# Kernel tuning notes

Hardware: AMD Instinct MI355X
Metric: run time of the kernel (lower is better)

The kernel has to match this reference:

```python
import jax, jax.numpy as jnp
import numpy as np
import math

B, N, E, D = 4, 8192, 1024, 64

def setup_inputs() -> dict:
    key = jax.random.key(0)
    kx, kq, kk, kv, ko = jax.random.split(key, 5)
    x = jax.random.normal(kx, (B, N, E), dtype=jnp.float32)
    # ImplicitLinear weights: hash-generated Rademacher-like values scaled by 1/sqrt(in_features).
    # We stand in with sign(normal) * scale, matching the statistics of v_mask_generative * scale.
    wq = jnp.sign(jax.random.normal(kq, (D, E), dtype=jnp.float32)) / math.sqrt(E)
    wk = jnp.sign(jax.random.normal(kk, (D, E), dtype=jnp.float32)) / math.sqrt(E)
    wv = jnp.sign(jax.random.normal(kv, (D, E), dtype=jnp.float32)) / math.sqrt(E)
    wo = jnp.sign(jax.random.normal(ko, (E, D), dtype=jnp.float32)) / math.sqrt(D)
    return {"x": x, "wq": wq, "wk": wk, "wv": wv, "wo": wo}

def reference(x, wq, wk, wv, wo):
    # Projections: ImplicitLinear computes x @ W.T with W shaped [out, in]
    Q = jnp.einsum('bne,de->bnd', x, wq)   # [B,N,D]
    K = jnp.einsum('bne,de->bnd', x, wk)   # [B,N,D]
    V = jnp.einsum('bne,de->bnd', x, wv)   # [B,N,D]
    # ground mode: linear attention, energy = K^T @ V  -> [B,D,D]
    energy = jnp.einsum('bnd,bne->bde', K, V)
    context = jnp.einsum('bnd,bde->bne', Q, energy)  # [B,N,D]
    context = context * jnp.asarray(math.sqrt(3.0 / D), dtype=context.dtype)
    out = jnp.einsum('bnd,ed->bne', context, wo)  # [B,N,E]
    return out
```

## Files before the change

### kernel.cpp

```cpp
#include <hip/hip_runtime.h>
#include <hip/hip_bf16.h>
#include <stdint.h>


typedef __bf16 bf16x8 __attribute__((ext_vector_type(8)));
typedef float  f32x4  __attribute__((ext_vector_type(4)));

#define MFMA_BF16(A, Bb, C) __builtin_amdgcn_mfma_f32_16x16x32_bf16(A, Bb, C, 0, 0, 0)

__global__ __launch_bounds__(128) void prep_kernel(
    const float* __restrict__ wq, const float* __restrict__ wk,
    const float* __restrict__ wv, const float* __restrict__ wo,
    __bf16* __restrict__ Wb)
{
    const int gid = blockIdx.x * 128 + threadIdx.x;
    const int e0  = gid * 8;
    const float* src = (e0 < 65536)  ? wq + e0
                     : (e0 < 131072) ? wk + (e0 - 65536)
                     : (e0 < 196608) ? wv + (e0 - 131072)
                                     : wo + (e0 - 196608);
    float w[8];
    *(float4*)&w[0] = *(const float4*)(src);
    *(float4*)&w[4] = *(const float4*)(src + 4);
    bf16x8 wb;
#pragma unroll
    for (int j = 0; j < 8; ++j) wb[j] = (__bf16)w[j];
    *(bf16x8*)&Wb[e0] = wb;
}

__global__ __launch_bounds__(256) void qkv_kernel(
    const float* __restrict__ x, const __bf16* __restrict__ Wb,
    float* __restrict__ Qf, float* __restrict__ Kf, float* __restrict__ Vf)
{
    const int tid  = threadIdx.x;
    const int lane = tid & 63;
    const int wid  = tid >> 6;
    const int lr   = lane & 15;
    const int kg   = lane >> 4;
    const int slab = blockIdx.x >> 1;
    const int c0   = (blockIdx.x & 1) * 96;
    const int row0 = slab * 64 + wid * 16;

    const float* xrow = &x[(size_t)(row0 + lr) * 1024 + kg * 8];

    f32x4 acc[6];
#pragma unroll
    for (int i = 0; i < 6; ++i) acc[i] = (f32x4){0.f, 0.f, 0.f, 0.f};

    float4 pa0, pa1, qa0, qa1;
    bf16x8 Bc[6], Bn[6];

#define LOAD_A(B0, B1, STP) {                                                  \
        const float* ap_ = xrow + (STP) * 32;                                  \
        B0 = *(const float4*)(ap_);                                            \
        B1 = *(const float4*)(ap_ + 4); }
#define LOAD_B(BARR, STP) {                                                    \
        _Pragma("unroll")                                                      \
        for (int bn_ = 0; bn_ < 6; ++bn_)                                      \
            BARR[bn_] = *(const bf16x8*)&Wb[(size_t)(c0 + bn_ * 16 + lr) * 1024 \
                                            + (STP) * 32 + kg * 8]; }
#define K1_STEP(S, A0_, A1_, BC, BN) {                                         \
        if ((S) + 1 < 32) LOAD_B(BN, (S) + 1);                                 \
        bf16x8 Ah_, Al_;                                                       \
        const float* fp_ = (const float*)&A0_;                                 \
        _Pragma("unroll")                                                      \
        for (int j_ = 0; j_ < 4; ++j_) {                                       \
            const unsigned int bb_ = __float_as_uint(fp_[j_]);                 \
            Ah_[j_] = __builtin_bit_cast(__bf16, (unsigned short)(bb_ >> 16)); \
            Al_[j_] = (__bf16)(fp_[j_] - __uint_as_float(bb_ & 0xffff0000u));  \
        }                                                                      \
        const float* gp_ = (const float*)&A1_;                                 \
        _Pragma("unroll")                                                      \
        for (int j_ = 0; j_ < 4; ++j_) {                                       \
            const unsigned int bb_ = __float_as_uint(gp_[j_]);                 \
            Ah_[4 + j_] = __builtin_bit_cast(__bf16, (unsigned short)(bb_ >> 16)); \
            Al_[4 + j_] = (__bf16)(gp_[j_] - __uint_as_float(bb_ & 0xffff0000u)); \
        }                                                                      \
        if ((S) + 2 < 32) LOAD_A(A0_, A1_, (S) + 2);                           \
        _Pragma("unroll")                                                      \
        for (int bn_ = 0; bn_ < 6; ++bn_) {                                    \
            acc[bn_] = MFMA_BF16(Ah_, BC[bn_], acc[bn_]);                      \
            acc[bn_] = MFMA_BF16(Al_, BC[bn_], acc[bn_]);                      \
        } }

    LOAD_A(pa0, pa1, 0);
    LOAD_A(qa0, qa1, 1);
    LOAD_B(Bc, 0);

    for (int s = 0; s < 32; s += 2) {
        K1_STEP(s,     pa0, pa1, Bc, Bn);
        K1_STEP(s + 1, qa0, qa1, Bn, Bc);
    }
#undef LOAD_A
#undef LOAD_B
#undef K1_STEP

#pragma unroll
    for (int bn = 0; bn < 6; ++bn) {
        const int col  = c0 + bn * 16 + lr;
        const int rowb = row0 + kg * 4;
        float* dst = (col < 64) ? Qf : (col < 128) ? Kf : Vf;
        const int cc = col & 63;
#pragma unroll
        for (int r = 0; r < 4; ++r)
            dst[(size_t)(rowb + r) * 64 + cc] = acc[bn][r];
    }
}

__global__ __launch_bounds__(256) void energy_partial_kernel(
    const float* __restrict__ Kf, const float* __restrict__ Vf,
    float* __restrict__ part)
{
    __shared__ float lK[64 * 64];
    __shared__ float lV[64 * 64];
    const int tid  = threadIdx.x;
    const int row0 = blockIdx.x * 64;

#pragma unroll
    for (int i = 0; i < 4; ++i) {
        const int idx = tid + i * 256;
        const int r   = idx >> 4;
        const int c4  = (idx & 15) << 2;
        *(float4*)&lK[r * 64 + c4] = *(const float4*)&Kf[(size_t)(row0 + r) * 64 + c4];
        *(float4*)&lV[r * 64 + c4] = *(const float4*)&Vf[(size_t)(row0 + r) * 64 + c4];
    }
    __syncthreads();

    const int d  = tid & 63;
    const int eb = (tid >> 6) * 16;
    float acc[16];
#pragma unroll
    for (int j = 0; j < 16; ++j) acc[j] = 0.f;

    for (int n = 0; n < 64; ++n) {
        const float kd = lK[n * 64 + d];
        const float4 v0 = *(const float4*)&lV[n * 64 + eb];
        const float4 v1 = *(const float4*)&lV[n * 64 + eb + 4];
        const float4 v2 = *(const float4*)&lV[n * 64 + eb + 8];
        const float4 v3 = *(const float4*)&lV[n * 64 + eb + 12];
        acc[0]  += kd * v0.x; acc[1]  += kd * v0.y; acc[2]  += kd * v0.z; acc[3]  += kd * v0.w;
        acc[4]  += kd * v1.x; acc[5]  += kd * v1.y; acc[6]  += kd * v1.z; acc[7]  += kd * v1.w;
        acc[8]  += kd * v2.x; acc[9]  += kd * v2.y; acc[10] += kd * v2.z; acc[11] += kd * v2.w;
        acc[12] += kd * v3.x; acc[13] += kd * v3.y; acc[14] += kd * v3.z; acc[15] += kd * v3.w;
    }
    float* p = part + (size_t)blockIdx.x * 4096 + d * 64 + eb;
#pragma unroll
    for (int i = 0; i < 4; ++i)
        *(float4*)&p[i * 4] = make_float4(acc[i*4], acc[i*4+1], acc[i*4+2], acc[i*4+3]);
}

__global__ __launch_bounds__(256) void energy_reduce_kernel(
    const float* __restrict__ part, __bf16* __restrict__ Eth, __bf16* __restrict__ Etl)
{
    const int b    = blockIdx.x >> 4;
    const int elem = ((blockIdx.x & 15) << 8) + threadIdx.x;
    float s = 0.f;
#pragma unroll 8
    for (int c = 0; c < 128; ++c)
        s += part[(size_t)(b * 128 + c) * 4096 + elem];
    s *= 0.2165063509461097f;
    const int d = elem >> 6, e = elem & 63;
    const __bf16 h = (__bf16)s;
    const __bf16 l = (__bf16)(s - (float)h);
    const size_t o = (size_t)b * 4096 + e * 64 + d;
    Eth[o] = h; Etl[o] = l;
}

__global__ __launch_bounds__(256) void out_kernel(
    const float* __restrict__ Qf,
    const __bf16* __restrict__ Eth, const __bf16* __restrict__ Etl,
    const __bf16* __restrict__ Wob, float* __restrict__ out)
{
    __shared__ float ct[4][16 * 68];

    const int tid  = threadIdx.x;
    const int lane = tid & 63;
    const int wid  = tid >> 6;
    const int lr   = lane & 15;
    const int kg   = lane >> 4;
    const int slab = blockIdx.x >> 1;
    const int c0   = (blockIdx.x & 1) * 512;
    const int row0 = slab * 64 + wid * 16;
    const int b    = blockIdx.x >> 8;

    bf16x8 Qh[2], Ql[2];
#pragma unroll
    for (int ks = 0; ks < 2; ++ks) {
        float qv[8];
        const float* src = &Qf[(size_t)(row0 + lr) * 64 + ks * 32 + kg * 8];
        *(float4*)&qv[0] = *(const float4*)(src);
        *(float4*)&qv[4] = *(const float4*)(src + 4);
#pragma unroll
        for (int j = 0; j < 8; ++j) {
            const unsigned int bb = __float_as_uint(qv[j]);
            Qh[ks][j] = __builtin_bit_cast(__bf16, (unsigned short)(bb >> 16));
            Ql[ks][j] = (__bf16)(qv[j] - __uint_as_float(bb & 0xffff0000u));
        }
    }

    f32x4 cacc[4];
#pragma unroll
    for (int i = 0; i < 4; ++i) cacc[i] = (f32x4){0.f, 0.f, 0.f, 0.f};
#pragma unroll
    for (int ks = 0; ks < 2; ++ks) {
#pragma unroll
        for (int eb = 0; eb < 4; ++eb) {
            const int e = eb * 16 + lr;
            const bf16x8 Bh = *(const bf16x8*)&Eth[(size_t)b * 4096 + e * 64 + ks * 32 + kg * 8];
            const bf16x8 Bl = *(const bf16x8*)&Etl[(size_t)b * 4096 + e * 64 + ks * 32 + kg * 8];
            cacc[eb] = MFMA_BF16(Qh[ks], Bh, cacc[eb]);
            cacc[eb] = MFMA_BF16(Qh[ks], Bl, cacc[eb]);
            cacc[eb] = MFMA_BF16(Ql[ks], Bh, cacc[eb]);
        }
    }

#pragma unroll
    for (int eb = 0; eb < 4; ++eb)
#pragma unroll
        for (int r = 0; r < 4; ++r)
            ct[wid][(kg * 4 + r) * 68 + eb * 16 + lr] = cacc[eb][r];
    asm volatile("s_waitcnt lgkmcnt(0)" ::: "memory");

    bf16x8 Ah[2], Al[2];
#pragma unroll
    for (int ks = 0; ks < 2; ++ks) {
        float f[8];
#pragma unroll
        for (int i = 0; i < 2; ++i)
            *(float4*)&f[i * 4] = *(const float4*)&ct[wid][lr * 68 + ks * 32 + kg * 8 + i * 4];
#pragma unroll
        for (int j = 0; j < 8; ++j) {
            const unsigned int bb = __float_as_uint(f[j]);
            Ah[ks][j] = __builtin_bit_cast(__bf16, (unsigned short)(bb >> 16));
            Al[ks][j] = (__bf16)(f[j] - __uint_as_float(bb & 0xffff0000u));
        }
    }

    for (int g = 0; g < 8; ++g) {
        f32x4 oacc[4];
#pragma unroll
        for (int i = 0; i < 4; ++i) oacc[i] = (f32x4){0.f, 0.f, 0.f, 0.f};
#pragma unroll
        for (int ks = 0; ks < 2; ++ks) {
#pragma unroll
            for (int bn = 0; bn < 4; ++bn) {
                const int col = c0 + g * 64 + bn * 16 + lr;
                const bf16x8 Bw = *(const bf16x8*)&Wob[(size_t)col * 64 + ks * 32 + kg * 8];
                oacc[bn] = MFMA_BF16(Ah[ks], Bw, oacc[bn]);
                oacc[bn] = MFMA_BF16(Al[ks], Bw, oacc[bn]);
            }
        }
#pragma unroll
        for (int bn = 0; bn < 4; ++bn)
#pragma unroll
            for (int r = 0; r < 4; ++r)
                __builtin_nontemporal_store(oacc[bn][r],
                    &out[(size_t)(row0 + kg * 4 + r) * 1024 + c0 + g * 64 + bn * 16 + lr]);
    }
}

extern "C" void kernel_launch(void* const* d_in, const int* in_sizes, int n_in,
                              void* d_out, int out_size, void* d_ws, size_t ws_size,
                              hipStream_t stream)
{
    const float* x  = (const float*)d_in[0];
    const float* wq = (const float*)d_in[1];
    const float* wk = (const float*)d_in[2];
    const float* wv = (const float*)d_in[3];
    const float* wo = (const float*)d_in[4];
    float* out = (float*)d_out;

    char* ws = (char*)d_ws;
    float*  Qf   = (float*)(ws);
    float*  Kf   = (float*)(ws + 8388608);
    float*  Vf   = (float*)(ws + 16777216);
    float*  part = (float*)(ws + 25165824);
    __bf16* Wb   = (__bf16*)(ws + 33554432);
    __bf16* Wob  = Wb + 196608;
    __bf16* Eth  = (__bf16*)(ws + 34603008);
    __bf16* Etl  = (__bf16*)(ws + 34635776);

    prep_kernel<<<256, 128, 0, stream>>>(wq, wk, wv, wo, Wb);
    qkv_kernel<<<1024, 256, 0, stream>>>(x, Wb, Qf, Kf, Vf);
    energy_partial_kernel<<<512, 256, 0, stream>>>(Kf, Vf, part);
    energy_reduce_kernel<<<64, 256, 0, stream>>>(part, Eth, Etl);
    out_kernel<<<1024, 256, 0, stream>>>(Qf, Eth, Etl, Wob, out);
}
```

Baseline: 362.5 us.

## Precompose energy with output weights and stage x tiles through LDS in QKV

```diff
diff --git a/kernel.cpp b/kernel.cpp
--- a/kernel.cpp
+++ b/kernel.cpp
@@ -4,9 +4,25 @@
 
 
 typedef __bf16 bf16x8 __attribute__((ext_vector_type(8)));
+typedef __bf16 bf16x4 __attribute__((ext_vector_type(4)));
 typedef float  f32x4  __attribute__((ext_vector_type(4)));
 
 #define MFMA_BF16(A, Bb, C) __builtin_amdgcn_mfma_f32_16x16x32_bf16(A, Bb, C, 0, 0, 0)
+
+__device__ __forceinline__ void gload_lds16(const void* g, void* l) {
+    __builtin_amdgcn_global_load_lds(
+        (const __attribute__((address_space(1))) unsigned int*)g,
+        (__attribute__((address_space(3))) unsigned int*)l, 16, 0, 0);
+}
+
+__device__ __forceinline__ void split8(const float* f, bf16x8& h, bf16x8& l) {
+#pragma unroll
+    for (int j = 0; j < 8; ++j) {
+        const unsigned int u = __float_as_uint(f[j]);
+        h[j] = __builtin_bit_cast(__bf16, (unsigned short)(u >> 16));
+        l[j] = (__bf16)(f[j] - __uint_as_float(u & 0xffff0000u));
+    }
+}
 
 __global__ __launch_bounds__(128) void prep_kernel(
     const float* __restrict__ wq, const float* __restrict__ wk,
@@ -28,82 +44,83 @@
     *(bf16x8*)&Wb[e0] = wb;
 }
 
-__global__ __launch_bounds__(256) void qkv_kernel(
+__global__ __launch_bounds__(512, 4) void qkv_kernel(
     const float* __restrict__ x, const __bf16* __restrict__ Wb,
     float* __restrict__ Qf, float* __restrict__ Kf, float* __restrict__ Vf)
 {
+    __shared__ float xt[2][64 * 64];
+
     const int tid  = threadIdx.x;
     const int lane = tid & 63;
     const int wid  = tid >> 6;
     const int lr   = lane & 15;
     const int kg   = lane >> 4;
-    const int slab = blockIdx.x >> 1;
-    const int c0   = (blockIdx.x & 1) * 96;
-    const int row0 = slab * 64 + wid * 16;
-
-    const float* xrow = &x[(size_t)(row0 + lr) * 1024 + kg * 8];
+    const int wr   = wid >> 1;
+    const int wc   = wid & 1;
+    const int row0 = blockIdx.x * 64;
+
+    const int q0 = wid * 2;
+    const int s0 = q0 * 64 + lane;
+    const int s1 = s0 + 64;
+    const int r0 = s0 >> 4, c0 = s0 & 15;
+    const int r1 = s1 >> 4, c1 = s1 & 15;
+    const float* src0 = x + (size_t)(row0 + r0) * 1024 + (c0 ^ (r0 & 7)) * 4;
+    const float* src1 = x + (size_t)(row0 + r1) * 1024 + (c1 ^ (r1 & 7)) * 4;
+
+#define STAGE(stp, buf) {                                                      \
+        gload_lds16(src0 + (stp) * 64, (char*)&xt[buf][0] + (q0 + 0) * 1024);  \
+        gload_lds16(src1 + (stp) * 64, (char*)&xt[buf][0] + (q0 + 1) * 1024); }
 
     f32x4 acc[6];
 #pragma unroll
     for (int i = 0; i < 6; ++i) acc[i] = (f32x4){0.f, 0.f, 0.f, 0.f};
 
-    float4 pa0, pa1, qa0, qa1;
-    bf16x8 Bc[6], Bn[6];
-
-#define LOAD_A(B0, B1, STP) {                                                  \
-        const float* ap_ = xrow + (STP) * 32;                                  \
-        B0 = *(const float4*)(ap_);                                            \
-        B1 = *(const float4*)(ap_ + 4); }
-#define LOAD_B(BARR, STP) {                                                    \
-        _Pragma("unroll")                                                      \
-        for (int bn_ = 0; bn_ < 6; ++bn_)                                      \
-            BARR[bn_] = *(const bf16x8*)&Wb[(size_t)(c0 + bn_ * 16 + lr) * 1024 \
-                                            + (STP) * 32 + kg * 8]; }
-#define K1_STEP(S, A0_, A1_, BC, BN) {                                         \
-        if ((S) + 1 < 32) LOAD_B(BN, (S) + 1);                                 \
-        bf16x8 Ah_, Al_;                                                       \
-        const float* fp_ = (const float*)&A0_;                                 \
-        _Pragma("unroll")                                                      \
-        for (int j_ = 0; j_ < 4; ++j_) {                                       \
-            const unsigned int bb_ = __float_as_uint(fp_[j_]);                 \
-            Ah_[j_] = __builtin_bit_cast(__bf16, (unsigned short)(bb_ >> 16)); \
-            Al_[j_] = (__bf16)(fp_[j_] - __uint_as_float(bb_ & 0xffff0000u));  \
-        }                                                                      \
-        const float* gp_ = (const float*)&A1_;                                 \
-        _Pragma("unroll")                                                      \
-        for (int j_ = 0; j_ < 4; ++j_) {                                       \
-            const unsigned int bb_ = __float_as_uint(gp_[j_]);                 \
-            Ah_[4 + j_] = __builtin_bit_cast(__bf16, (unsigned short)(bb_ >> 16)); \
-            Al_[4 + j_] = (__bf16)(gp_[j_] - __uint_as_float(bb_ & 0xffff0000u)); \
-        }                                                                      \
-        if ((S) + 2 < 32) LOAD_A(A0_, A1_, (S) + 2);                           \
-        _Pragma("unroll")                                                      \
-        for (int bn_ = 0; bn_ < 6; ++bn_) {                                    \
-            acc[bn_] = MFMA_BF16(Ah_, BC[bn_], acc[bn_]);                      \
-            acc[bn_] = MFMA_BF16(Al_, BC[bn_], acc[bn_]);                      \
-        } }
-
-    LOAD_A(pa0, pa1, 0);
-    LOAD_A(qa0, qa1, 1);
-    LOAD_B(Bc, 0);
-
-    for (int s = 0; s < 32; s += 2) {
-        K1_STEP(s,     pa0, pa1, Bc, Bn);
-        K1_STEP(s + 1, qa0, qa1, Bn, Bc);
-    }
-#undef LOAD_A
-#undef LOAD_B
-#undef K1_STEP
-
-#pragma unroll
-    for (int bn = 0; bn < 6; ++bn) {
-        const int col  = c0 + bn * 16 + lr;
-        const int rowb = row0 + kg * 4;
+    STAGE(0, 0);
+
+    const int ar  = wr * 16 + lr;
+    const int am  = ar & 7;
+
+    for (int step = 0; step < 16; ++step) {
+        const int cur = step & 1;
+        __syncthreads();
+
+        bf16x8 Bw[2][6];
+#pragma unroll
+        for (int ks = 0; ks < 2; ++ks)
+#pragma unroll
+            for (int n = 0; n < 6; ++n)
+                Bw[ks][n] = *(const bf16x8*)&Wb[(size_t)(wc * 96 + n * 16 + lr) * 1024
+                                                + step * 64 + ks * 32 + kg * 8];
+        if (step + 1 < 16) STAGE(step + 1, cur ^ 1);
+
+        bf16x8 Ah[2], Al[2];
+#pragma unroll
+        for (int ks = 0; ks < 2; ++ks) {
+            const int g0 = ks * 8 + kg * 2;
+            float f[8];
+            *(f32x4*)&f[0] = *(const f32x4*)&xt[cur][ar * 64 + ((g0    ) ^ am) * 4];
+            *(f32x4*)&f[4] = *(const f32x4*)&xt[cur][ar * 64 + ((g0 + 1) ^ am) * 4];
+            split8(f, Ah[ks], Al[ks]);
+        }
+#pragma unroll
+        for (int ks = 0; ks < 2; ++ks)
+#pragma unroll
+            for (int n = 0; n < 6; ++n) {
+                acc[n] = MFMA_BF16(Ah[ks], Bw[ks][n], acc[n]);
+                acc[n] = MFMA_BF16(Al[ks], Bw[ks][n], acc[n]);
+            }
+    }
+#undef STAGE
+
+#pragma unroll
+    for (int n = 0; n < 6; ++n) {
+        const int col  = wc * 96 + n * 16 + lr;
+        const int rowb = row0 + wr * 16 + kg * 4;
         float* dst = (col < 64) ? Qf : (col < 128) ? Kf : Vf;
         const int cc = col & 63;
 #pragma unroll
         for (int r = 0; r < 4; ++r)
-            dst[(size_t)(rowb + r) * 64 + cc] = acc[bn][r];
+            dst[(size_t)(rowb + r) * 64 + cc] = acc[n][r];
     }
 }
 
@@ -150,7 +167,7 @@
 }
 
 __global__ __launch_bounds__(256) void energy_reduce_kernel(
-    const float* __restrict__ part, __bf16* __restrict__ Eth, __bf16* __restrict__ Etl)
+    const float* __restrict__ part, __bf16* __restrict__ Eh, __bf16* __restrict__ El)
 {
     const int b    = blockIdx.x >> 4;
     const int elem = ((blockIdx.x & 15) << 8) + threadIdx.x;
@@ -159,103 +176,127 @@
     for (int c = 0; c < 128; ++c)
         s += part[(size_t)(b * 128 + c) * 4096 + elem];
     s *= 0.2165063509461097f;
-    const int d = elem >> 6, e = elem & 63;
     const __bf16 h = (__bf16)s;
     const __bf16 l = (__bf16)(s - (float)h);
-    const size_t o = (size_t)b * 4096 + e * 64 + d;
-    Eth[o] = h; Etl[o] = l;
-}
-
-__global__ __launch_bounds__(256) void out_kernel(
-    const float* __restrict__ Qf,
-    const __bf16* __restrict__ Eth, const __bf16* __restrict__ Etl,
-    const __bf16* __restrict__ Wob, float* __restrict__ out)
-{
-    __shared__ float ct[4][16 * 68];
-
+    Eh[b * 4096 + elem] = h;
+    El[b * 4096 + elem] = l;
+}
+
+__global__ __launch_bounds__(256) void f_kernel(
+    const __bf16* __restrict__ Eh, const __bf16* __restrict__ El,
+    const __bf16* __restrict__ Wob,
+    __bf16* __restrict__ Fth, __bf16* __restrict__ Ftl)
+{
     const int tid  = threadIdx.x;
     const int lane = tid & 63;
     const int wid  = tid >> 6;
     const int lr   = lane & 15;
     const int kg   = lane >> 4;
-    const int slab = blockIdx.x >> 1;
-    const int c0   = (blockIdx.x & 1) * 512;
-    const int row0 = slab * 64 + wid * 16;
-    const int b    = blockIdx.x >> 8;
+    const int b    = blockIdx.x >> 2;
+    const int cg   = blockIdx.x & 3;
+
+    bf16x8 Ah[2], Al[2];
+#pragma unroll
+    for (int ks = 0; ks < 2; ++ks) {
+        const size_t o = (size_t)b * 4096 + (wid * 16 + lr) * 64 + ks * 32 + kg * 8;
+        Ah[ks] = *(const bf16x8*)&Eh[o];
+        Al[ks] = *(const bf16x8*)&El[o];
+    }
+
+#pragma unroll
+    for (int grp = 0; grp < 4; ++grp) {
+        f32x4 acc[4];
+#pragma unroll
+        for (int i = 0; i < 4; ++i) acc[i] = (f32x4){0.f, 0.f, 0.f, 0.f};
+        bf16x8 Bw[4][2];
+#pragma unroll
+        for (int n = 0; n < 4; ++n)
+#pragma unroll
+            for (int ks = 0; ks < 2; ++ks) {
+                const int col = cg * 256 + grp * 64 + n * 16 + lr;
+                Bw[n][ks] = *(const bf16x8*)&Wob[(size_t)col * 64 + ks * 32 + kg * 8];
+            }
+#pragma unroll
+        for (int ks = 0; ks < 2; ++ks)
+#pragma unroll
+            for (int n = 0; n < 4; ++n) {
+                acc[n] = MFMA_BF16(Ah[ks], Bw[n][ks], acc[n]);
+                acc[n] = MFMA_BF16(Al[ks], Bw[n][ks], acc[n]);
+            }
+#pragma unroll
+        for (int n = 0; n < 4; ++n) {
+            const int col = cg * 256 + grp * 64 + n * 16 + lr;
+            bf16x4 hv, lv;
+#pragma unroll
+            for (int r = 0; r < 4; ++r) {
+                const float v = acc[n][r];
+                hv[r] = (__bf16)v;
+                lv[r] = (__bf16)(v - (float)hv[r]);
+            }
+            const size_t o = (size_t)b * 65536 + (size_t)col * 64 + wid * 16 + kg * 4;
+            *(bf16x4*)&Fth[o] = hv;
+            *(bf16x4*)&Ftl[o] = lv;
+        }
+    }
+}
+
+__global__ __launch_bounds__(256, 4) void out_kernel(
+    const float* __restrict__ Qf,
+    const __bf16* __restrict__ Fth, const __bf16* __restrict__ Ftl,
+    float* __restrict__ out)
+{
+    const int tid    = threadIdx.x;
+    const int lane   = tid & 63;
+    const int wid    = tid >> 6;
+    const int lr     = lane & 15;
+    const int kg     = lane >> 4;
+    const int rowblk = blockIdx.x >> 2;
+    const int cg     = blockIdx.x & 3;
+    const int row0   = rowblk * 64 + wid * 16;
+    const int b      = rowblk >> 7;
 
     bf16x8 Qh[2], Ql[2];
-#pragma unroll
-    for (int ks = 0; ks < 2; ++ks) {
-        float qv[8];
-        const float* src = &Qf[(size_t)(row0 + lr) * 64 + ks * 32 + kg * 8];
-        *(float4*)&qv[0] = *(const float4*)(src);
-        *(float4*)&qv[4] = *(const float4*)(src + 4);
-#pragma unroll
-        for (int j = 0; j < 8; ++j) {
-            const unsigned int bb = __float_as_uint(qv[j]);
-            Qh[ks][j] = __builtin_bit_cast(__bf16, (unsigned short)(bb >> 16));
-            Ql[ks][j] = (__bf16)(qv[j] - __uint_as_float(bb & 0xffff0000u));
-        }
-    }
-
-    f32x4 cacc[4];
-#pragma unroll
-    for (int i = 0; i < 4; ++i) cacc[i] = (f32x4){0.f, 0.f, 0.f, 0.f};
-#pragma unroll
-    for (int ks = 0; ks < 2; ++ks) {
-#pragma unroll
-        for (int eb = 0; eb < 4; ++eb) {
-            const int e = eb * 16 + lr;
-            const bf16x8 Bh = *(const bf16x8*)&Eth[(size_t)b * 4096 + e * 64 + ks * 32 + kg * 8];
-            const bf16x8 Bl = *(const bf16x8*)&Etl[(size_t)b * 4096 + e * 64 + ks * 32 + kg * 8];
-            cacc[eb] = MFMA_BF16(Qh[ks], Bh, cacc[eb]);
-            cacc[eb] = MFMA_BF16(Qh[ks], Bl, cacc[eb]);
-            cacc[eb] = MFMA_BF16(Ql[ks], Bh, cacc[eb]);
-        }
-    }
-
-#pragma unroll
-    for (int eb = 0; eb < 4; ++eb)
-#pragma unroll
-        for (int r = 0; r < 4; ++r)
-            ct[wid][(kg * 4 + r) * 68 + eb * 16 + lr] = cacc[eb][r];
-    asm volatile("s_waitcnt lgkmcnt(0)" ::: "memory");
-
-    bf16x8 Ah[2], Al[2];
 #pragma unroll
     for (int ks = 0; ks < 2; ++ks) {
         float f[8];
-#pragma unroll
-        for (int i = 0; i < 2; ++i)
-            *(float4*)&f[i * 4] = *(const float4*)&ct[wid][lr * 68 + ks * 32 + kg * 8 + i * 4];
-#pragma unroll
-        for (int j = 0; j < 8; ++j) {
-            const unsigned int bb = __float_as_uint(f[j]);
-            Ah[ks][j] = __builtin_bit_cast(__bf16, (unsigned short)(bb >> 16));
-            Al[ks][j] = (__bf16)(f[j] - __uint_as_float(bb & 0xffff0000u));
+        const float* src = &Qf[(size_t)(row0 + lr) * 64 + ks * 32 + kg * 8];
+        *(float4*)&f[0] = *(const float4*)(src);
+        *(float4*)&f[4] = *(const float4*)(src + 4);
+        split8(f, Qh[ks], Ql[ks]);
+    }
+
+    const size_t fb = (size_t)b * 65536;
+#pragma unroll
+    for (int grp = 0; grp < 4; ++grp) {
+        bf16x8 Bh[4][2], Bl[4][2];
+#pragma unroll
+        for (int n = 0; n < 4; ++n)
+#pragma unroll
+            for (int ks = 0; ks < 2; ++ks) {
+                const size_t o = fb + (size_t)(cg * 256 + grp * 64 + n * 16 + lr) * 64
+                               + ks * 32 + kg * 8;
+                Bh[n][ks] = *(const bf16x8*)&Fth[o];
+                Bl[n][ks] = *(const bf16x8*)&Ftl[o];
+            }
+        f32x4 acc[4];
+#pragma unroll
+        for (int i = 0; i < 4; ++i) acc[i] = (f32x4){0.f, 0.f, 0.f, 0.f};
+#pragma unroll
+        for (int ks = 0; ks < 2; ++ks)
+#pragma unroll
+            for (int n = 0; n < 4; ++n) {
+                acc[n] = MFMA_BF16(Qh[ks], Bh[n][ks], acc[n]);
+                acc[n] = MFMA_BF16(Qh[ks], Bl[n][ks], acc[n]);
+                acc[n] = MFMA_BF16(Ql[ks], Bh[n][ks], acc[n]);
+            }
+#pragma unroll
+        for (int n = 0; n < 4; ++n) {
+            const int col = cg * 256 + grp * 64 + n * 16 + lr;
+#pragma unroll
+            for (int r = 0; r < 4; ++r)
+                __builtin_nontemporal_store(acc[n][r],
+                    &out[(size_t)(row0 + kg * 4 + r) * 1024 + col]);
         }
-    }
-
-    for (int g = 0; g < 8; ++g) {
-        f32x4 oacc[4];
-#pragma unroll
-        for (int i = 0; i < 4; ++i) oacc[i] = (f32x4){0.f, 0.f, 0.f, 0.f};
-#pragma unroll
-        for (int ks = 0; ks < 2; ++ks) {
-#pragma unroll
-            for (int bn = 0; bn < 4; ++bn) {
-                const int col = c0 + g * 64 + bn * 16 + lr;
-                const bf16x8 Bw = *(const bf16x8*)&Wob[(size_t)col * 64 + ks * 32 + kg * 8];
-                oacc[bn] = MFMA_BF16(Ah[ks], Bw, oacc[bn]);
-                oacc[bn] = MFMA_BF16(Al[ks], Bw, oacc[bn]);
-            }
-        }
-#pragma unroll
-        for (int bn = 0; bn < 4; ++bn)
-#pragma unroll
-            for (int r = 0; r < 4; ++r)
-                __builtin_nontemporal_store(oacc[bn][r],
-                    &out[(size_t)(row0 + kg * 4 + r) * 1024 + c0 + g * 64 + bn * 16 + lr]);
     }
 }
 
@@ -277,12 +318,15 @@
     float*  part = (float*)(ws + 25165824);
     __bf16* Wb   = (__bf16*)(ws + 33554432);
     __bf16* Wob  = Wb + 196608;
-    __bf16* Eth  = (__bf16*)(ws + 34603008);
-    __bf16* Etl  = (__bf16*)(ws + 34635776);
+    __bf16* Eh   = (__bf16*)(ws + 34078720);
+    __bf16* El   = (__bf16*)(ws + 34111488);
+    __bf16* Fth  = (__bf16*)(ws + 34144256);
+    __bf16* Ftl  = (__bf16*)(ws + 34668544);
 
     prep_kernel<<<256, 128, 0, stream>>>(wq, wk, wv, wo, Wb);
-    qkv_kernel<<<1024, 256, 0, stream>>>(x, Wb, Qf, Kf, Vf);
+    qkv_kernel<<<512, 512, 0, stream>>>(x, Wb, Qf, Kf, Vf);
     energy_partial_kernel<<<512, 256, 0, stream>>>(Kf, Vf, part);
-    energy_reduce_kernel<<<64, 256, 0, stream>>>(part, Eth, Etl);
-    out_kernel<<<1024, 256, 0, stream>>>(Qf, Eth, Etl, Wob, out);
-}
+    energy_reduce_kernel<<<64, 256, 0, stream>>>(part, Eh, El);
+    f_kernel<<<16, 256, 0, stream>>>(Eh, El, Wob, Fth, Ftl);
+    out_kernel<<<2048, 256, 0, stream>>>(Qf, Fth, Ftl, out);
+}
```

Result: slower. 371.0 us (+2.4%).
